# Kernel optimization log

Measured on AMD Instinct MI355X. Metric: run time of the kernel, lower is better.

## Reference

```python
import jax, jax.numpy as jnp
import numpy as np

N_NODES = 50000
N_EDGES = 600000
CLASSIC_DIM = 128
GRAPH_OUTPUT_DIM = 96
NUM_RELATIONS = 4


def setup_inputs() -> dict:
    key = jax.random.key(0)
    ks = jax.random.split(key, 10)
    x = jax.random.normal(ks[0], (N_NODES, CLASSIC_DIM), dtype=jnp.float32)
    edge_index = jax.random.randint(ks[1], (2, N_EDGES), 0, N_NODES, dtype=jnp.int64)
    edge_type = jax.random.randint(ks[2], (N_EDGES,), 0, NUM_RELATIONS, dtype=jnp.int64)
    s1 = 1.0 / np.sqrt(CLASSIC_DIM)
    W_root1 = jax.random.normal(ks[3], (CLASSIC_DIM, CLASSIC_DIM), dtype=jnp.float32) * s1
    W_rel1 = jax.random.normal(ks[4], (NUM_RELATIONS, CLASSIC_DIM, CLASSIC_DIM), dtype=jnp.float32) * s1
    b1 = jnp.zeros((CLASSIC_DIM,), dtype=jnp.float32)
    W_root2 = jax.random.normal(ks[5], (CLASSIC_DIM, GRAPH_OUTPUT_DIM), dtype=jnp.float32) * s1
    W_rel2 = jax.random.normal(ks[6], (NUM_RELATIONS, CLASSIC_DIM, GRAPH_OUTPUT_DIM), dtype=jnp.float32) * s1
    b2 = jnp.zeros((GRAPH_OUTPUT_DIM,), dtype=jnp.float32)
    return {"classic_features": x, "edge_index": edge_index, "edge_type": edge_type,
            "W_root1": W_root1, "W_rel1": W_rel1, "b1": b1,
            "W_root2": W_root2, "W_rel2": W_rel2, "b2": b2}


def _rgcn_layer(x, edge_index, edge_type, W_root, W_rel, b):
    # RGCN: h_i = W_root x_i + b + sum_r (1/deg_{i,r}) * W_r * sum_{j in N_r(i)} x_j
    # Aggregate-then-transform (valid by linearity) to keep the matmul small.
    src, dst = edge_index[0], edge_index[1]
    msgs = x[src]  # [E, d_in] irregular gather
    out = x @ W_root + b
    n = x.shape[0]
    num_rel = W_rel.shape[0]
    for r in range(num_rel):  # small fixed loop over relation types
        mask = (edge_type == r).astype(x.dtype)  # [E]
        agg = jax.ops.segment_sum(msgs * mask[:, None], dst, num_segments=n)  # [N, d_in]
        deg = jax.ops.segment_sum(mask, dst, num_segments=n)  # [N]
        agg = agg / jnp.maximum(deg, 1.0)[:, None]  # mean per relation (PyG default norm)
        out = out + agg @ W_rel[r]
    return out


def reference(classic_features, edge_index, edge_type, W_root1, W_rel1, b1, W_root2, W_rel2, b2):
    h = _rgcn_layer(classic_features, edge_index, edge_type, W_root1, W_rel1, b1)
    h = jax.nn.relu(h)
    # dropout(0.2) is identity in eval mode
    out = _rgcn_layer(h, edge_index, edge_type, W_root2, W_rel2, b2)
    return out
```

## Files before the change

kernel.cpp:

```cpp
#include <hip/hip_runtime.h>

#define DIM_IN 128
#define NREL 4
#define KTOT (DIM_IN + NREL * DIM_IN)
#define SCAN_CHUNK 1024

typedef __attribute__((ext_vector_type(8))) short short8;
typedef __attribute__((ext_vector_type(4))) float floatx4;

__device__ inline unsigned short f2bf(float f) {
    union { float f; unsigned int i; } c;
    c.f = f;
    unsigned int r = c.i + 0x7FFF + ((c.i >> 16) & 1);
    return (unsigned short)(r >> 16);
}
__device__ inline float bf2f(unsigned short u) {
    union { unsigned int i; float f; } c;
    c.i = ((unsigned int)u) << 16;
    return c.f;
}

__device__ inline void gload16_lds(const void* g, void* l) {
    __builtin_amdgcn_global_load_lds((const __attribute__((address_space(1))) unsigned int*)g,
                                     (__attribute__((address_space(3))) unsigned int*)l,
                                     16, 0, 0);
}

__global__ __launch_bounds__(256) void prep_kernel(
    const float* __restrict__ x, unsigned short* __restrict__ xb, int n4,
    const float* __restrict__ Wroot1, const float* __restrict__ Wrel1,
    unsigned short* __restrict__ Wt1,
    const float* __restrict__ Wroot2, const float* __restrict__ Wrel2,
    unsigned short* __restrict__ Wt2,
    const int* __restrict__ ei, const int* __restrict__ et,
    int* __restrict__ counts, int E) {
    int t = blockIdx.x * 256 + threadIdx.x;
    if (t < n4) {
        float4 v = ((const float4*)x)[t];
        ushort4 o;
        o.x = f2bf(v.x); o.y = f2bf(v.y); o.z = f2bf(v.z); o.w = f2bf(v.w);
        ((ushort4*)xb)[t] = o;
    }
    if (t < (128 + 96) * KTOT) {
        if (t < 128 * KTOT) {
            int n = t / KTOT, k = t - n * KTOT;
            float v = (k < DIM_IN) ? Wroot1[(size_t)k * 128 + n]
                                   : Wrel1[(size_t)(k - DIM_IN) * 128 + n];
            Wt1[t] = f2bf(v);
        } else {
            int t2 = t - 128 * KTOT;
            int n = t2 / KTOT, k = t2 - n * KTOT;
            float v = (k < DIM_IN) ? Wroot2[(size_t)k * 96 + n]
                                   : Wrel2[(size_t)(k - DIM_IN) * 96 + n];
            Wt2[t2] = f2bf(v);
        }
    }
    if (t < E) {
        atomicAdd(&counts[(size_t)ei[E + t] * NREL + et[t]], 1);
    }
}

__device__ int block_exscan256(int v) {
    __shared__ int tmp[256];
    int t = threadIdx.x;
    tmp[t] = v;
    __syncthreads();
    for (int d = 1; d < 256; d <<= 1) {
        int add = (t >= d) ? tmp[t - d] : 0;
        __syncthreads();
        tmp[t] += add;
        __syncthreads();
    }
    return tmp[t] - v;
}

__global__ __launch_bounds__(256) void scanA_kernel(const int* __restrict__ counts,
                                                    int* __restrict__ chunkTot, int nb) {
    int base = blockIdx.x * SCAN_CHUNK + threadIdx.x * 4;
    int s = 0;
#pragma unroll
    for (int i = 0; i < 4; i++) {
        int idx = base + i;
        s += (idx < nb) ? counts[idx] : 0;
    }
    __shared__ int red[256];
    red[threadIdx.x] = s;
    __syncthreads();
    for (int d = 128; d > 0; d >>= 1) {
        if (threadIdx.x < d) red[threadIdx.x] += red[threadIdx.x + d];
        __syncthreads();
    }
    if (threadIdx.x == 0) chunkTot[blockIdx.x] = red[0];
}

__global__ __launch_bounds__(256) void scanB_kernel(const int* __restrict__ chunkTot,
                                                    int* __restrict__ chunkBase, int nChunks) {
    int t = threadIdx.x;
    int v = (t < nChunks) ? chunkTot[t] : 0;
    int ex = block_exscan256(v);
    if (t < nChunks) chunkBase[t] = ex;
}

__global__ __launch_bounds__(256) void scanC_kernel(const int* __restrict__ counts,
                                                    const int* __restrict__ chunkBase,
                                                    int* __restrict__ offs,
                                                    int* __restrict__ cursor, int nb) {
    int base = blockIdx.x * SCAN_CHUNK + threadIdx.x * 4;
    int c[4], s = 0;
#pragma unroll
    for (int i = 0; i < 4; i++) {
        int idx = base + i;
        c[i] = (idx < nb) ? counts[idx] : 0;
        s += c[i];
    }
    int pos = block_exscan256(s) + chunkBase[blockIdx.x];
#pragma unroll
    for (int i = 0; i < 4; i++) {
        int idx = base + i;
        if (idx < nb) {
            offs[idx] = pos;
            cursor[idx] = pos;
        }
        pos += c[i];
    }
}

__global__ void place_kernel(const int* __restrict__ ei, const int* __restrict__ et,
                             int* __restrict__ cursor, int* __restrict__ csr, int E) {
    int e = blockIdx.x * 256 + threadIdx.x;
    if (e >= E) return;
    int b = ei[E + e] * NREL + et[e];
    int p = atomicAdd(&cursor[b], 1);
    csr[p] = ei[e];
}

__global__ __launch_bounds__(256) void agg_kernel(
    const unsigned short* __restrict__ feat, const int* __restrict__ csr,
    const int* __restrict__ offs, const int* __restrict__ counts,
    unsigned short* __restrict__ agg, int nb) {
    int l16 = threadIdx.x & 15;
    int g = (blockIdx.x * 256 + threadIdx.x) >> 4;
    if (g >= nb) return;
    int start = offs[g];
    int cnt = counts[g];
    float acc[8];
#pragma unroll
    for (int j = 0; j < 8; j++) acc[j] = 0.f;
    for (int base = 0; base < cnt; base += 16) {
        int m = cnt - base;
        if (m > 16) m = 16;
        int pick = (l16 < m) ? l16 : (m - 1);
        int idx = csr[start + base + pick];
        for (int j = 0; j < m; j++) {
            int s = __shfl(idx, j, 16);
            short8 u = *(const short8*)(feat + (size_t)s * DIM_IN + l16 * 8);
#pragma unroll
            for (int c = 0; c < 8; c++) acc[c] += bf2f((unsigned short)u[c]);
        }
    }
    float sc = (cnt > 0) ? (1.0f / (float)cnt) : 0.f;
    short8 o;
#pragma unroll
    for (int j = 0; j < 8; j++) o[j] = (short)f2bf(acc[j] * sc);
    *(short8*)(agg + (size_t)g * DIM_IN + l16 * 8) = o;
}

template <int NOUT, bool STORE_BF16_RELU>
__global__ __launch_bounds__(256) void mfma_gemm_kernel(
    const unsigned short* __restrict__ xb,
    const unsigned short* __restrict__ agg,
    const unsigned short* __restrict__ Wt,
    const float* __restrict__ bias,
    void* __restrict__ outp,
    int N) {
    constexpr int NT = NOUT / 32;
    constexpr int ACH = 128 * 8;
    constexpr int BCH = NOUT * 8;
    constexpr int APAN = 128 * 32;
    constexpr int BPAN = NOUT * 32;
    __shared__ unsigned short sA[2 * APAN];
    __shared__ unsigned short sB[2 * BPAN];
    const int t = threadIdx.x;
    const int w = t >> 6;
    const int lane = t & 63;
    const int q = lane >> 4;
    const int l15 = lane & 15;
    const int wm = w >> 1, wn = w & 1;
    const int m0 = blockIdx.x * 128;

    floatx4 acc[4][NT];
#pragma unroll
    for (int mt = 0; mt < 4; mt++)
#pragma unroll
        for (int nt = 0; nt < NT; nt++) acc[mt][nt] = (floatx4)0.f;

    for (int ks = 0; ks < KTOT / 64; ks++) {
        const int k0 = ks * 64;
#pragma unroll
        for (int r = 0; r < ACH / 256; r++) {
            int idx = t + r * 256;
            int panel = idx >> 9;
            int rem = idx & 511;
            int row = rem >> 2, ch = rem & 3;
            int rowg = m0 + row;
            if (rowg >= N) rowg = N - 1;
            int col = panel * 32 + ch * 8;
            const unsigned short* gp =
                (k0 < DIM_IN)
                    ? (xb + (size_t)rowg * DIM_IN + k0 + col)
                    : (agg + (size_t)rowg * (NREL * DIM_IN) + (k0 - DIM_IN) + col);
            gload16_lds(gp, sA + (size_t)idx * 8);
        }
#pragma unroll
        for (int r = 0; r < BCH / 256; r++) {
            int idx = t + r * 256;
            int panel = idx / (NOUT * 4);
            int rem = idx - panel * (NOUT * 4);
            int nrow = rem >> 2, ch = rem & 3;
            const unsigned short* gp = Wt + (size_t)nrow * KTOT + k0 + panel * 32 + ch * 8;
            gload16_lds(gp, sB + (size_t)idx * 8);
        }
        __syncthreads();
#pragma unroll
        for (int s = 0; s < 2; s++) {
            short8 aF[4], bF[NT];
#pragma unroll
            for (int mt = 0; mt < 4; mt++)
                aF[mt] = *(const short8*)(sA + s * APAN +
                                          (size_t)(wm * 64 + mt * 16 + l15) * 32 + q * 8);
#pragma unroll
            for (int nt = 0; nt < NT; nt++)
                bF[nt] = *(const short8*)(sB + s * BPAN +
                                          (size_t)(wn * (NOUT / 2) + nt * 16 + l15) * 32 + q * 8);
#pragma unroll
            for (int mt = 0; mt < 4; mt++)
#pragma unroll
                for (int nt = 0; nt < NT; nt++)
                    acc[mt][nt] = __builtin_amdgcn_mfma_f32_16x16x32_bf16(aF[mt], bF[nt],
                                                                          acc[mt][nt], 0, 0, 0);
        }
        __syncthreads();
    }

#pragma unroll
    for (int nt = 0; nt < NT; nt++) {
        int colg = wn * (NOUT / 2) + nt * 16 + l15;
        float bv = bias[colg];
#pragma unroll
        for (int mt = 0; mt < 4; mt++) {
            int rbase = m0 + wm * 64 + mt * 16 + q * 4;
#pragma unroll
            for (int r = 0; r < 4; r++) {
                int grow = rbase + r;
                if (grow < N) {
                    float v = acc[mt][nt][r] + bv;
                    if (STORE_BF16_RELU) {
                        v = fmaxf(v, 0.f);
                        ((unsigned short*)outp)[(size_t)grow * NOUT + colg] = f2bf(v);
                    } else {
                        ((float*)outp)[(size_t)grow * NOUT + colg] = v;
                    }
                }
            }
        }
    }
}

extern "C" void kernel_launch(void* const* d_in, const int* in_sizes, int n_in,
                              void* d_out, int out_size, void* d_ws, size_t ws_size,
                              hipStream_t stream) {
    const float* x = (const float*)d_in[0];
    const int* ei = (const int*)d_in[1];
    const int* et = (const int*)d_in[2];
    const float* Wroot1 = (const float*)d_in[3];
    const float* Wrel1 = (const float*)d_in[4];
    const float* b1 = (const float*)d_in[5];
    const float* Wroot2 = (const float*)d_in[6];
    const float* Wrel2 = (const float*)d_in[7];
    const float* b2 = (const float*)d_in[8];
    float* out = (float*)d_out;

    int N = in_sizes[0] / DIM_IN;
    int E = in_sizes[2];
    int nb = N * NREL;
    int nChunks = (nb + SCAN_CHUNK - 1) / SCAN_CHUNK;

    char* p = (char*)d_ws;
    unsigned short* xb = (unsigned short*)p;   p += (size_t)N * DIM_IN * 2;
    unsigned short* hb = (unsigned short*)p;   p += (size_t)N * DIM_IN * 2;
    unsigned short* agg = (unsigned short*)p;  p += (size_t)nb * DIM_IN * 2;
    unsigned short* Wt1 = (unsigned short*)p;  p += (size_t)128 * KTOT * 2;
    unsigned short* Wt2 = (unsigned short*)p;  p += (size_t)96 * KTOT * 2;
    int* counts = (int*)p;                     p += (size_t)nb * 4;
    int* offs = (int*)p;                       p += (size_t)nb * 4;
    int* cursor = (int*)p;                     p += (size_t)nb * 4;
    int* chunkTot = (int*)p;                   p += 256 * 4;
    int* chunkBase = (int*)p;                  p += 256 * 4;
    int* csr = (int*)p;                        p += (size_t)E * 4;
    if ((size_t)(p - (char*)d_ws) > ws_size) return;

    int n4 = N * DIM_IN / 4;
    int prepWork = n4;
    if (prepWork < E) prepWork = E;
    if (prepWork < (128 + 96) * KTOT) prepWork = (128 + 96) * KTOT;

    hipMemsetAsync(counts, 0, (size_t)nb * sizeof(int), stream);
    prep_kernel<<<(prepWork + 255) / 256, 256, 0, stream>>>(
        x, xb, n4, Wroot1, Wrel1, Wt1, Wroot2, Wrel2, Wt2, ei, et, counts, E);
    scanA_kernel<<<nChunks, 256, 0, stream>>>(counts, chunkTot, nb);
    scanB_kernel<<<1, 256, 0, stream>>>(chunkTot, chunkBase, nChunks);
    scanC_kernel<<<nChunks, 256, 0, stream>>>(counts, chunkBase, offs, cursor, nb);
    place_kernel<<<(E + 255) / 256, 256, 0, stream>>>(ei, et, cursor, csr, E);

    int gAgg = (nb * 16 + 255) / 256;
    int gB = (N + 127) / 128;
    agg_kernel<<<gAgg, 256, 0, stream>>>(xb, csr, offs, counts, agg, nb);
    mfma_gemm_kernel<128, true><<<gB, 256, 0, stream>>>(xb, agg, Wt1, b1, hb, N);
    agg_kernel<<<gAgg, 256, 0, stream>>>(hb, csr, offs, counts, agg, nb);
    mfma_gemm_kernel<96, false><<<gB, 256, 0, stream>>>(hb, agg, Wt2, b2, out, N);
}
```

Baseline: 262.3 us.

## Switch RGCN layers to transform-then-aggregate with per-node gather over packed CSR

Each layer now first multiplies node features by the concatenated root and relation weights (N x 128 times 128 x 5C), then a gather kernel sums each destination's neighbours from the transformed relation slices, scaled by the inverse per-relation degree, on top of the root term. Edge relation ids are packed into the CSR source index so one pass per node covers all relations. The place atomics now advance the offset array in place, and the prefix shifted by one element recovers segment starts. This removes the N*4*128 aggregated intermediate and the long-K GEMM, but the GEMM output grows to 5C columns per node, and gathers read C-wide rows with fewer active lanes when C is 96.

```diff
diff --git a/kernel.cpp b/kernel.cpp
--- a/kernel.cpp
+++ b/kernel.cpp
@@ -2,8 +2,8 @@
 
 #define DIM_IN 128
 #define NREL 4
-#define KTOT (DIM_IN + NREL * DIM_IN)
 #define SCAN_CHUNK 1024
+#define SRC_MASK 0xFFFFF
 
 typedef __attribute__((ext_vector_type(8))) short short8;
 typedef __attribute__((ext_vector_type(4))) float floatx4;
@@ -41,17 +41,23 @@
         o.x = f2bf(v.x); o.y = f2bf(v.y); o.z = f2bf(v.z); o.w = f2bf(v.w);
         ((ushort4*)xb)[t] = o;
     }
-    if (t < (128 + 96) * KTOT) {
-        if (t < 128 * KTOT) {
-            int n = t / KTOT, k = t - n * KTOT;
-            float v = (k < DIM_IN) ? Wroot1[(size_t)k * 128 + n]
-                                   : Wrel1[(size_t)(k - DIM_IN) * 128 + n];
+    if (t < (640 + 480) * 128) {
+        if (t < 640 * 128) {
+            int n = t >> 7, k = t & 127;
+            float v = (n < 128) ? Wroot1[(size_t)k * 128 + n]
+                                : Wrel1[(size_t)((((n - 128) >> 7) * 128) + k) * 128 +
+                                        ((n - 128) & 127)];
             Wt1[t] = f2bf(v);
         } else {
-            int t2 = t - 128 * KTOT;
-            int n = t2 / KTOT, k = t2 - n * KTOT;
-            float v = (k < DIM_IN) ? Wroot2[(size_t)k * 96 + n]
-                                   : Wrel2[(size_t)(k - DIM_IN) * 96 + n];
+            int t2 = t - 640 * 128;
+            int n = t2 >> 7, k = t2 & 127;
+            float v;
+            if (n < 96) {
+                v = Wroot2[(size_t)k * 96 + n];
+            } else {
+                int q = n - 96, r = q / 96, c = q - r * 96;
+                v = Wrel2[(size_t)(r * 128 + k) * 96 + c];
+            }
             Wt2[t2] = f2bf(v);
         }
     }
@@ -94,17 +100,18 @@
 }
 
 __global__ __launch_bounds__(256) void scanB_kernel(const int* __restrict__ chunkTot,
-                                                    int* __restrict__ chunkBase, int nChunks) {
+                                                    int* __restrict__ chunkBase, int nChunks,
+                                                    int* __restrict__ curM1) {
     int t = threadIdx.x;
     int v = (t < nChunks) ? chunkTot[t] : 0;
     int ex = block_exscan256(v);
     if (t < nChunks) chunkBase[t] = ex;
+    if (t == 0) curM1[0] = 0;
 }
 
 __global__ __launch_bounds__(256) void scanC_kernel(const int* __restrict__ counts,
                                                     const int* __restrict__ chunkBase,
-                                                    int* __restrict__ offs,
-                                                    int* __restrict__ cursor, int nb) {
+                                                    int* __restrict__ cur, int nb) {
     int base = blockIdx.x * SCAN_CHUNK + threadIdx.x * 4;
     int c[4], s = 0;
 #pragma unroll
@@ -117,76 +124,59 @@
 #pragma unroll
     for (int i = 0; i < 4; i++) {
         int idx = base + i;
-        if (idx < nb) {
-            offs[idx] = pos;
-            cursor[idx] = pos;
-        }
+        if (idx < nb) cur[idx] = pos;
         pos += c[i];
     }
 }
 
 __global__ void place_kernel(const int* __restrict__ ei, const int* __restrict__ et,
-                             int* __restrict__ cursor, int* __restrict__ csr, int E) {
+                             int* __restrict__ cur, int* __restrict__ csr, int E) {
     int e = blockIdx.x * 256 + threadIdx.x;
     if (e >= E) return;
-    int b = ei[E + e] * NREL + et[e];
-    int p = atomicAdd(&cursor[b], 1);
-    csr[p] = ei[e];
-}
-
-__global__ __launch_bounds__(256) void agg_kernel(
-    const unsigned short* __restrict__ feat, const int* __restrict__ csr,
-    const int* __restrict__ offs, const int* __restrict__ counts,
-    unsigned short* __restrict__ agg, int nb) {
-    int l16 = threadIdx.x & 15;
-    int g = (blockIdx.x * 256 + threadIdx.x) >> 4;
-    if (g >= nb) return;
-    int start = offs[g];
-    int cnt = counts[g];
-    float acc[8];
-#pragma unroll
-    for (int j = 0; j < 8; j++) acc[j] = 0.f;
-    for (int base = 0; base < cnt; base += 16) {
-        int m = cnt - base;
-        if (m > 16) m = 16;
-        int pick = (l16 < m) ? l16 : (m - 1);
-        int idx = csr[start + base + pick];
-        for (int j = 0; j < m; j++) {
-            int s = __shfl(idx, j, 16);
-            short8 u = *(const short8*)(feat + (size_t)s * DIM_IN + l16 * 8);
-#pragma unroll
-            for (int c = 0; c < 8; c++) acc[c] += bf2f((unsigned short)u[c]);
-        }
-    }
-    float sc = (cnt > 0) ? (1.0f / (float)cnt) : 0.f;
-    short8 o;
-#pragma unroll
-    for (int j = 0; j < 8; j++) o[j] = (short)f2bf(acc[j] * sc);
-    *(short8*)(agg + (size_t)g * DIM_IN + l16 * 8) = o;
-}
-
-template <int NOUT, bool STORE_BF16_RELU>
-__global__ __launch_bounds__(256) void mfma_gemm_kernel(
-    const unsigned short* __restrict__ xb,
-    const unsigned short* __restrict__ agg,
+    int r = et[e];
+    int b = ei[E + e] * NREL + r;
+    int p = atomicAdd(&cur[b], 1);
+    csr[p] = ei[e] | (r << 20);
+}
+
+template <int CH, int NTOT>
+__global__ __launch_bounds__(256) void gemm_tf_kernel(
+    const unsigned short* __restrict__ A,
     const unsigned short* __restrict__ Wt,
     const float* __restrict__ bias,
-    void* __restrict__ outp,
+    unsigned short* __restrict__ y,
     int N) {
-    constexpr int NT = NOUT / 32;
-    constexpr int ACH = 128 * 8;
-    constexpr int BCH = NOUT * 8;
-    constexpr int APAN = 128 * 32;
-    constexpr int BPAN = NOUT * 32;
-    __shared__ unsigned short sA[2 * APAN];
-    __shared__ unsigned short sB[2 * BPAN];
+    constexpr int NT = CH / 32;
+    constexpr int BCHP = CH * 4;
+    __shared__ unsigned short sA[128 * 128];
+    __shared__ unsigned short sB[CH * 128];
     const int t = threadIdx.x;
     const int w = t >> 6;
     const int lane = t & 63;
     const int q = lane >> 4;
     const int l15 = lane & 15;
     const int wm = w >> 1, wn = w & 1;
-    const int m0 = blockIdx.x * 128;
+    const int m0 = blockIdx.y * 128;
+    const int c0 = blockIdx.x * CH;
+
+#pragma unroll
+    for (int r = 0; r < 8; r++) {
+        int idx = t + r * 256;
+        int panel = idx >> 9, rem = idx & 511;
+        int row = rem >> 2, ch = rem & 3;
+        int rowg = m0 + row;
+        if (rowg >= N) rowg = N - 1;
+        gload16_lds(A + (size_t)rowg * 128 + panel * 32 + ch * 8, sA + (size_t)idx * 8);
+    }
+#pragma unroll
+    for (int r = 0; r < (CH * 16) / 256; r++) {
+        int idx = t + r * 256;
+        int panel = idx / BCHP, rem = idx - panel * BCHP;
+        int nrow = rem >> 2, ch = rem & 3;
+        gload16_lds(Wt + (size_t)(c0 + nrow) * 128 + panel * 32 + ch * 8,
+                    sB + (size_t)idx * 8);
+    }
+    __syncthreads();
 
     floatx4 acc[4][NT];
 #pragma unroll
@@ -194,74 +184,114 @@
 #pragma unroll
         for (int nt = 0; nt < NT; nt++) acc[mt][nt] = (floatx4)0.f;
 
-    for (int ks = 0; ks < KTOT / 64; ks++) {
-        const int k0 = ks * 64;
-#pragma unroll
-        for (int r = 0; r < ACH / 256; r++) {
-            int idx = t + r * 256;
-            int panel = idx >> 9;
-            int rem = idx & 511;
-            int row = rem >> 2, ch = rem & 3;
-            int rowg = m0 + row;
-            if (rowg >= N) rowg = N - 1;
-            int col = panel * 32 + ch * 8;
-            const unsigned short* gp =
-                (k0 < DIM_IN)
-                    ? (xb + (size_t)rowg * DIM_IN + k0 + col)
-                    : (agg + (size_t)rowg * (NREL * DIM_IN) + (k0 - DIM_IN) + col);
-            gload16_lds(gp, sA + (size_t)idx * 8);
-        }
-#pragma unroll
-        for (int r = 0; r < BCH / 256; r++) {
-            int idx = t + r * 256;
-            int panel = idx / (NOUT * 4);
-            int rem = idx - panel * (NOUT * 4);
-            int nrow = rem >> 2, ch = rem & 3;
-            const unsigned short* gp = Wt + (size_t)nrow * KTOT + k0 + panel * 32 + ch * 8;
-            gload16_lds(gp, sB + (size_t)idx * 8);
-        }
-        __syncthreads();
-#pragma unroll
-        for (int s = 0; s < 2; s++) {
-            short8 aF[4], bF[NT];
-#pragma unroll
-            for (int mt = 0; mt < 4; mt++)
-                aF[mt] = *(const short8*)(sA + s * APAN +
-                                          (size_t)(wm * 64 + mt * 16 + l15) * 32 + q * 8);
+#pragma unroll
+    for (int s = 0; s < 4; s++) {
+        short8 aF[4], bF[NT];
+#pragma unroll
+        for (int mt = 0; mt < 4; mt++)
+            aF[mt] = *(const short8*)(sA + s * 4096 + (size_t)(wm * 64 + mt * 16 + l15) * 32 + q * 8);
+#pragma unroll
+        for (int nt = 0; nt < NT; nt++)
+            bF[nt] = *(const short8*)(sB + s * (CH * 32) +
+                                      (size_t)(wn * (CH / 2) + nt * 16 + l15) * 32 + q * 8);
+#pragma unroll
+        for (int mt = 0; mt < 4; mt++)
 #pragma unroll
             for (int nt = 0; nt < NT; nt++)
-                bF[nt] = *(const short8*)(sB + s * BPAN +
-                                          (size_t)(wn * (NOUT / 2) + nt * 16 + l15) * 32 + q * 8);
-#pragma unroll
-            for (int mt = 0; mt < 4; mt++)
-#pragma unroll
-                for (int nt = 0; nt < NT; nt++)
-                    acc[mt][nt] = __builtin_amdgcn_mfma_f32_16x16x32_bf16(aF[mt], bF[nt],
-                                                                          acc[mt][nt], 0, 0, 0);
-        }
-        __syncthreads();
+                acc[mt][nt] =
+                    __builtin_amdgcn_mfma_f32_16x16x32_bf16(aF[mt], bF[nt], acc[mt][nt], 0, 0, 0);
     }
 
 #pragma unroll
     for (int nt = 0; nt < NT; nt++) {
-        int colg = wn * (NOUT / 2) + nt * 16 + l15;
-        float bv = bias[colg];
+        int colc = wn * (CH / 2) + nt * 16 + l15;
+        int colg = c0 + colc;
+        float bv = (blockIdx.x == 0) ? bias[colc] : 0.f;
 #pragma unroll
         for (int mt = 0; mt < 4; mt++) {
             int rbase = m0 + wm * 64 + mt * 16 + q * 4;
 #pragma unroll
             for (int r = 0; r < 4; r++) {
                 int grow = rbase + r;
-                if (grow < N) {
-                    float v = acc[mt][nt][r] + bv;
-                    if (STORE_BF16_RELU) {
-                        v = fmaxf(v, 0.f);
-                        ((unsigned short*)outp)[(size_t)grow * NOUT + colg] = f2bf(v);
-                    } else {
-                        ((float*)outp)[(size_t)grow * NOUT + colg] = v;
-                    }
-                }
+                if (grow < N)
+                    y[(size_t)grow * NTOT + colg] = f2bf(acc[mt][nt][r] + bv);
             }
+        }
+    }
+}
+
+template <int NTOT, int ROOTC, bool RELU_BF16>
+__global__ __launch_bounds__(256) void gather_kernel(
+    const unsigned short* __restrict__ y, const int* __restrict__ csr,
+    const int* __restrict__ cur, void* __restrict__ outp, int N) {
+    constexpr int AL = ROOTC / 8;
+    const int l = threadIdx.x & 15;
+    const int dst = (blockIdx.x * 256 + threadIdx.x) >> 4;
+    if (dst >= N) return;
+    const int g0 = dst * NREL;
+    int o0 = cur[g0 - 1], o1 = cur[g0], o2 = cur[g0 + 1], o3 = cur[g0 + 2], o4 = cur[g0 + 3];
+    float sc0 = (o1 > o0) ? 1.f / (float)(o1 - o0) : 0.f;
+    float sc1 = (o2 > o1) ? 1.f / (float)(o2 - o1) : 0.f;
+    float sc2 = (o3 > o2) ? 1.f / (float)(o3 - o2) : 0.f;
+    float sc3 = (o4 > o3) ? 1.f / (float)(o4 - o3) : 0.f;
+    int tot = o4 - o0;
+
+    float acc[8];
+    if (l < AL) {
+        short8 rt = *(const short8*)(y + (size_t)dst * NTOT + l * 8);
+#pragma unroll
+        for (int c = 0; c < 8; c++) acc[c] = bf2f((unsigned short)rt[c]);
+    } else {
+#pragma unroll
+        for (int c = 0; c < 8; c++) acc[c] = 0.f;
+    }
+
+    for (int b0 = 0; b0 < tot; b0 += 16) {
+        int m = tot - b0;
+        if (m > 16) m = 16;
+        int pick = (l < m) ? l : (m - 1);
+        int pv = csr[o0 + b0 + pick];
+        int j = 0;
+        for (; j + 1 < m; j += 2) {
+            int v0 = __shfl(pv, j, 16);
+            int v1 = __shfl(pv, j + 1, 16);
+            int s0 = v0 & SRC_MASK, r0 = v0 >> 20;
+            int s1 = v1 & SRC_MASK, r1 = v1 >> 20;
+            float f0 = (r0 == 0) ? sc0 : (r0 == 1) ? sc1 : (r0 == 2) ? sc2 : sc3;
+            float f1 = (r1 == 0) ? sc0 : (r1 == 1) ? sc1 : (r1 == 2) ? sc2 : sc3;
+            if (l < AL) {
+                short8 u0 = *(const short8*)(y + (size_t)s0 * NTOT + ROOTC + r0 * ROOTC + l * 8);
+                short8 u1 = *(const short8*)(y + (size_t)s1 * NTOT + ROOTC + r1 * ROOTC + l * 8);
+#pragma unroll
+                for (int c = 0; c < 8; c++) acc[c] += f0 * bf2f((unsigned short)u0[c]);
+#pragma unroll
+                for (int c = 0; c < 8; c++) acc[c] += f1 * bf2f((unsigned short)u1[c]);
+            }
+        }
+        if (j < m) {
+            int v0 = __shfl(pv, j, 16);
+            int s0 = v0 & SRC_MASK, r0 = v0 >> 20;
+            float f0 = (r0 == 0) ? sc0 : (r0 == 1) ? sc1 : (r0 == 2) ? sc2 : sc3;
+            if (l < AL) {
+                short8 u0 = *(const short8*)(y + (size_t)s0 * NTOT + ROOTC + r0 * ROOTC + l * 8);
+#pragma unroll
+                for (int c = 0; c < 8; c++) acc[c] += f0 * bf2f((unsigned short)u0[c]);
+            }
+        }
+    }
+
+    if (l < AL) {
+        if (RELU_BF16) {
+            short8 o;
+#pragma unroll
+            for (int c = 0; c < 8; c++) o[c] = (short)f2bf(fmaxf(acc[c], 0.f));
+            *(short8*)((unsigned short*)outp + (size_t)dst * ROOTC + l * 8) = o;
+        } else {
+            float4 a = make_float4(acc[0], acc[1], acc[2], acc[3]);
+            float4 b = make_float4(acc[4], acc[5], acc[6], acc[7]);
+            float4* op = (float4*)((float*)outp + (size_t)dst * ROOTC + l * 8);
+            op[0] = a;
+            op[1] = b;
         }
     }
 }
@@ -286,36 +316,37 @@
     int nChunks = (nb + SCAN_CHUNK - 1) / SCAN_CHUNK;
 
     char* p = (char*)d_ws;
-    unsigned short* xb = (unsigned short*)p;   p += (size_t)N * DIM_IN * 2;
-    unsigned short* hb = (unsigned short*)p;   p += (size_t)N * DIM_IN * 2;
-    unsigned short* agg = (unsigned short*)p;  p += (size_t)nb * DIM_IN * 2;
-    unsigned short* Wt1 = (unsigned short*)p;  p += (size_t)128 * KTOT * 2;
-    unsigned short* Wt2 = (unsigned short*)p;  p += (size_t)96 * KTOT * 2;
+    unsigned short* xb = (unsigned short*)p;   p += (size_t)N * 128 * 2;
+    unsigned short* hb = (unsigned short*)p;   p += (size_t)N * 128 * 2;
+    unsigned short* y1 = (unsigned short*)p;   p += (size_t)N * 640 * 2;
+    unsigned short* y2 = (unsigned short*)p;   p += (size_t)N * 480 * 2;
+    unsigned short* Wt1 = (unsigned short*)p;  p += (size_t)640 * 128 * 2;
+    unsigned short* Wt2 = (unsigned short*)p;  p += (size_t)480 * 128 * 2;
     int* counts = (int*)p;                     p += (size_t)nb * 4;
-    int* offs = (int*)p;                       p += (size_t)nb * 4;
-    int* cursor = (int*)p;                     p += (size_t)nb * 4;
+    int* curBuf = (int*)p;                     p += ((size_t)nb + 1) * 4;
     int* chunkTot = (int*)p;                   p += 256 * 4;
     int* chunkBase = (int*)p;                  p += 256 * 4;
     int* csr = (int*)p;                        p += (size_t)E * 4;
     if ((size_t)(p - (char*)d_ws) > ws_size) return;
-
-    int n4 = N * DIM_IN / 4;
+    int* cur = curBuf + 1;
+
+    int n4 = N * 128 / 4;
     int prepWork = n4;
     if (prepWork < E) prepWork = E;
-    if (prepWork < (128 + 96) * KTOT) prepWork = (128 + 96) * KTOT;
+    if (prepWork < (640 + 480) * 128) prepWork = (640 + 480) * 128;
 
     hipMemsetAsync(counts, 0, (size_t)nb * sizeof(int), stream);
     prep_kernel<<<(prepWork + 255) / 256, 256, 0, stream>>>(
         x, xb, n4, Wroot1, Wrel1, Wt1, Wroot2, Wrel2, Wt2, ei, et, counts, E);
     scanA_kernel<<<nChunks, 256, 0, stream>>>(counts, chunkTot, nb);
-    scanB_kernel<<<1, 256, 0, stream>>>(chunkTot, chunkBase, nChunks);
-    scanC_kernel<<<nChunks, 256, 0, stream>>>(counts, chunkBase, offs, cursor, nb);
-    place_kernel<<<(E + 255) / 256, 256, 0, stream>>>(ei, et, cursor, csr, E);
-
-    int gAgg = (nb * 16 + 255) / 256;
-    int gB = (N + 127) / 128;
-    agg_kernel<<<gAgg, 256, 0, stream>>>(xb, csr, offs, counts, agg, nb);
-    mfma_gemm_kernel<128, true><<<gB, 256, 0, stream>>>(xb, agg, Wt1, b1, hb, N);
-    agg_kernel<<<gAgg, 256, 0, stream>>>(hb, csr, offs, counts, agg, nb);
-    mfma_gemm_kernel<96, false><<<gB, 256, 0, stream>>>(hb, agg, Wt2, b2, out, N);
-}
+    scanB_kernel<<<1, 256, 0, stream>>>(chunkTot, chunkBase, nChunks, curBuf);
+    scanC_kernel<<<nChunks, 256, 0, stream>>>(counts, chunkBase, cur, nb);
+    place_kernel<<<(E + 255) / 256, 256, 0, stream>>>(ei, et, cur, csr, E);
+
+    int gM = (N + 127) / 128;
+    int gG = (N * 16 + 255) / 256;
+    gemm_tf_kernel<128, 640><<<dim3(5, gM), 256, 0, stream>>>(xb, Wt1, b1, y1, N);
+    gather_kernel<640, 128, true><<<gG, 256, 0, stream>>>(y1, csr, cur, hb, N);
+    gemm_tf_kernel<96, 480><<<dim3(5, gM), 256, 0, stream>>>(hb, Wt2, b2, y2, N);
+    gather_kernel<480, 96, false><<<gG, 256, 0, stream>>>(y2, csr, cur, out, N);
+}
```

Result: slower. 299.4 us (+14.2%).

## Fuse neighbor aggregation into GEMM A-tile loading and drop agg buffer

Applied to the files above, without the earlier changes.

Removes the separate aggregation kernels and the intermediate per-relation aggregate buffer. The GEMM now builds the relation A-tiles on the fly by gathering neighbor rows through the CSR and averaging them in registers before writing to LDS. After place_kernel the post-atomic cursor array doubles as the end-offset array, with a leading zero slot so cur[g-1] gives the start, which removes the separate offs buffer. This trades a global write and read of the aggregate for irregular gathers done inside the GEMM with only 8 lanes per row. That leaves far fewer threads doing the gathers, exposes their latency, and puts the gather on the GEMM's critical path.

```diff
diff --git a/kernel.cpp b/kernel.cpp
--- a/kernel.cpp
+++ b/kernel.cpp
@@ -41,19 +41,17 @@
         o.x = f2bf(v.x); o.y = f2bf(v.y); o.z = f2bf(v.z); o.w = f2bf(v.w);
         ((ushort4*)xb)[t] = o;
     }
-    if (t < (128 + 96) * KTOT) {
-        if (t < 128 * KTOT) {
-            int n = t / KTOT, k = t - n * KTOT;
-            float v = (k < DIM_IN) ? Wroot1[(size_t)k * 128 + n]
-                                   : Wrel1[(size_t)(k - DIM_IN) * 128 + n];
-            Wt1[t] = f2bf(v);
-        } else {
-            int t2 = t - 128 * KTOT;
-            int n = t2 / KTOT, k = t2 - n * KTOT;
-            float v = (k < DIM_IN) ? Wroot2[(size_t)k * 96 + n]
-                                   : Wrel2[(size_t)(k - DIM_IN) * 96 + n];
-            Wt2[t2] = f2bf(v);
-        }
+    if (t < 128 * KTOT) {
+        int n = t / KTOT, k = t - n * KTOT;
+        float v = (k < DIM_IN) ? Wroot1[(size_t)k * 128 + n]
+                               : Wrel1[(size_t)(k - DIM_IN) * 128 + n];
+        Wt1[t] = f2bf(v);
+    }
+    if (t < 96 * KTOT) {
+        int n = t / KTOT, k = t - n * KTOT;
+        float v = (k < DIM_IN) ? Wroot2[(size_t)k * 96 + n]
+                               : Wrel2[(size_t)(k - DIM_IN) * 96 + n];
+        Wt2[t] = f2bf(v);
     }
     if (t < E) {
         atomicAdd(&counts[(size_t)ei[E + t] * NREL + et[t]], 1);
@@ -94,17 +92,18 @@
 }
 
 __global__ __launch_bounds__(256) void scanB_kernel(const int* __restrict__ chunkTot,
-                                                    int* __restrict__ chunkBase, int nChunks) {
+                                                    int* __restrict__ chunkBase, int nChunks,
+                                                    int* __restrict__ curM1) {
     int t = threadIdx.x;
     int v = (t < nChunks) ? chunkTot[t] : 0;
     int ex = block_exscan256(v);
     if (t < nChunks) chunkBase[t] = ex;
+    if (t == 0) curM1[0] = 0;
 }
 
 __global__ __launch_bounds__(256) void scanC_kernel(const int* __restrict__ counts,
                                                     const int* __restrict__ chunkBase,
-                                                    int* __restrict__ offs,
-                                                    int* __restrict__ cursor, int nb) {
+                                                    int* __restrict__ cur, int nb) {
     int base = blockIdx.x * SCAN_CHUNK + threadIdx.x * 4;
     int c[4], s = 0;
 #pragma unroll
@@ -117,65 +116,30 @@
 #pragma unroll
     for (int i = 0; i < 4; i++) {
         int idx = base + i;
-        if (idx < nb) {
-            offs[idx] = pos;
-            cursor[idx] = pos;
-        }
+        if (idx < nb) cur[idx] = pos;
         pos += c[i];
     }
 }
 
 __global__ void place_kernel(const int* __restrict__ ei, const int* __restrict__ et,
-                             int* __restrict__ cursor, int* __restrict__ csr, int E) {
+                             int* __restrict__ cur, int* __restrict__ csr, int E) {
     int e = blockIdx.x * 256 + threadIdx.x;
     if (e >= E) return;
     int b = ei[E + e] * NREL + et[e];
-    int p = atomicAdd(&cursor[b], 1);
+    int p = atomicAdd(&cur[b], 1);
     csr[p] = ei[e];
 }
 
-__global__ __launch_bounds__(256) void agg_kernel(
-    const unsigned short* __restrict__ feat, const int* __restrict__ csr,
-    const int* __restrict__ offs, const int* __restrict__ counts,
-    unsigned short* __restrict__ agg, int nb) {
-    int l16 = threadIdx.x & 15;
-    int g = (blockIdx.x * 256 + threadIdx.x) >> 4;
-    if (g >= nb) return;
-    int start = offs[g];
-    int cnt = counts[g];
-    float acc[8];
-#pragma unroll
-    for (int j = 0; j < 8; j++) acc[j] = 0.f;
-    for (int base = 0; base < cnt; base += 16) {
-        int m = cnt - base;
-        if (m > 16) m = 16;
-        int pick = (l16 < m) ? l16 : (m - 1);
-        int idx = csr[start + base + pick];
-        for (int j = 0; j < m; j++) {
-            int s = __shfl(idx, j, 16);
-            short8 u = *(const short8*)(feat + (size_t)s * DIM_IN + l16 * 8);
-#pragma unroll
-            for (int c = 0; c < 8; c++) acc[c] += bf2f((unsigned short)u[c]);
-        }
-    }
-    float sc = (cnt > 0) ? (1.0f / (float)cnt) : 0.f;
-    short8 o;
-#pragma unroll
-    for (int j = 0; j < 8; j++) o[j] = (short)f2bf(acc[j] * sc);
-    *(short8*)(agg + (size_t)g * DIM_IN + l16 * 8) = o;
-}
-
 template <int NOUT, bool STORE_BF16_RELU>
-__global__ __launch_bounds__(256) void mfma_gemm_kernel(
+__global__ __launch_bounds__(256) void gemm_fused_kernel(
     const unsigned short* __restrict__ xb,
-    const unsigned short* __restrict__ agg,
     const unsigned short* __restrict__ Wt,
+    const int* __restrict__ csr,
+    const int* __restrict__ cur,
     const float* __restrict__ bias,
     void* __restrict__ outp,
     int N) {
     constexpr int NT = NOUT / 32;
-    constexpr int ACH = 128 * 8;
-    constexpr int BCH = NOUT * 8;
     constexpr int APAN = 128 * 32;
     constexpr int BPAN = NOUT * 32;
     __shared__ unsigned short sA[2 * APAN];
@@ -187,6 +151,8 @@
     const int l15 = lane & 15;
     const int wm = w >> 1, wn = w & 1;
     const int m0 = blockIdx.x * 128;
+    const int grp = t >> 3;
+    const int gl = t & 7;
 
     floatx4 acc[4][NT];
 #pragma unroll
@@ -196,29 +162,52 @@
 
     for (int ks = 0; ks < KTOT / 64; ks++) {
         const int k0 = ks * 64;
-#pragma unroll
-        for (int r = 0; r < ACH / 256; r++) {
-            int idx = t + r * 256;
-            int panel = idx >> 9;
-            int rem = idx & 511;
-            int row = rem >> 2, ch = rem & 3;
-            int rowg = m0 + row;
-            if (rowg >= N) rowg = N - 1;
-            int col = panel * 32 + ch * 8;
-            const unsigned short* gp =
-                (k0 < DIM_IN)
-                    ? (xb + (size_t)rowg * DIM_IN + k0 + col)
-                    : (agg + (size_t)rowg * (NREL * DIM_IN) + (k0 - DIM_IN) + col);
-            gload16_lds(gp, sA + (size_t)idx * 8);
+        if (k0 < DIM_IN) {
+#pragma unroll
+            for (int r = 0; r < 4; r++) {
+                int idx = t + r * 256;
+                int panel = idx >> 9, rem = idx & 511;
+                int row = rem >> 2, ch = rem & 3;
+                int rowg = m0 + row;
+                if (rowg >= N) rowg = N - 1;
+                gload16_lds(xb + (size_t)rowg * DIM_IN + k0 + panel * 32 + ch * 8,
+                            sA + (size_t)idx * 8);
+            }
+        } else {
+            const int koff = k0 - DIM_IN;
+            const int rel = koff >> 7;
+            const int kbase = koff & 127;
+#pragma unroll
+            for (int p = 0; p < 4; p++) {
+                int row = p * 32 + grp;
+                int dstg = m0 + row;
+                if (dstg >= N) dstg = N - 1;
+                int g = dstg * NREL + rel;
+                int s0 = cur[g - 1], e0 = cur[g];
+                float facc[8];
+#pragma unroll
+                for (int c = 0; c < 8; c++) facc[c] = 0.f;
+                for (int i = s0; i < e0; i++) {
+                    int src = csr[i];
+                    short8 u = *(const short8*)(xb + (size_t)src * DIM_IN + kbase + gl * 8);
+#pragma unroll
+                    for (int c = 0; c < 8; c++) facc[c] += bf2f((unsigned short)u[c]);
+                }
+                float sc = (e0 > s0) ? (1.0f / (float)(e0 - s0)) : 0.f;
+                short8 o;
+#pragma unroll
+                for (int c = 0; c < 8; c++) o[c] = (short)f2bf(facc[c] * sc);
+                *(short8*)(sA + (gl >> 2) * APAN + (size_t)row * 32 + (gl & 3) * 8) = o;
+            }
         }
 #pragma unroll
-        for (int r = 0; r < BCH / 256; r++) {
+        for (int r = 0; r < (NOUT * 8) / 256; r++) {
             int idx = t + r * 256;
             int panel = idx / (NOUT * 4);
             int rem = idx - panel * (NOUT * 4);
             int nrow = rem >> 2, ch = rem & 3;
-            const unsigned short* gp = Wt + (size_t)nrow * KTOT + k0 + panel * 32 + ch * 8;
-            gload16_lds(gp, sB + (size_t)idx * 8);
+            gload16_lds(Wt + (size_t)nrow * KTOT + k0 + panel * 32 + ch * 8,
+                        sB + (size_t)idx * 8);
         }
         __syncthreads();
 #pragma unroll
@@ -288,34 +277,30 @@
     char* p = (char*)d_ws;
     unsigned short* xb = (unsigned short*)p;   p += (size_t)N * DIM_IN * 2;
     unsigned short* hb = (unsigned short*)p;   p += (size_t)N * DIM_IN * 2;
-    unsigned short* agg = (unsigned short*)p;  p += (size_t)nb * DIM_IN * 2;
     unsigned short* Wt1 = (unsigned short*)p;  p += (size_t)128 * KTOT * 2;
     unsigned short* Wt2 = (unsigned short*)p;  p += (size_t)96 * KTOT * 2;
     int* counts = (int*)p;                     p += (size_t)nb * 4;
-    int* offs = (int*)p;                       p += (size_t)nb * 4;
-    int* cursor = (int*)p;                     p += (size_t)nb * 4;
+    int* curBuf = (int*)p;                     p += ((size_t)nb + 1) * 4;
     int* chunkTot = (int*)p;                   p += 256 * 4;
     int* chunkBase = (int*)p;                  p += 256 * 4;
     int* csr = (int*)p;                        p += (size_t)E * 4;
     if ((size_t)(p - (char*)d_ws) > ws_size) return;
+    int* cur = curBuf + 1;
 
     int n4 = N * DIM_IN / 4;
     int prepWork = n4;
     if (prepWork < E) prepWork = E;
-    if (prepWork < (128 + 96) * KTOT) prepWork = (128 + 96) * KTOT;
+    if (prepWork < 128 * KTOT) prepWork = 128 * KTOT;
 
     hipMemsetAsync(counts, 0, (size_t)nb * sizeof(int), stream);
     prep_kernel<<<(prepWork + 255) / 256, 256, 0, stream>>>(
         x, xb, n4, Wroot1, Wrel1, Wt1, Wroot2, Wrel2, Wt2, ei, et, counts, E);
     scanA_kernel<<<nChunks, 256, 0, stream>>>(counts, chunkTot, nb);
-    scanB_kernel<<<1, 256, 0, stream>>>(chunkTot, chunkBase, nChunks);
-    scanC_kernel<<<nChunks, 256, 0, stream>>>(counts, chunkBase, offs, cursor, nb);
-    place_kernel<<<(E + 255) / 256, 256, 0, stream>>>(ei, et, cursor, csr, E);
-
-    int gAgg = (nb * 16 + 255) / 256;
+    scanB_kernel<<<1, 256, 0, stream>>>(chunkTot, chunkBase, nChunks, curBuf);
+    scanC_kernel<<<nChunks, 256, 0, stream>>>(counts, chunkBase, cur, nb);
+    place_kernel<<<(E + 255) / 256, 256, 0, stream>>>(ei, et, cur, csr, E);
+
     int gB = (N + 127) / 128;
-    agg_kernel<<<gAgg, 256, 0, stream>>>(xb, csr, offs, counts, agg, nb);
-    mfma_gemm_kernel<128, true><<<gB, 256, 0, stream>>>(xb, agg, Wt1, b1, hb, N);
-    agg_kernel<<<gAgg, 256, 0, stream>>>(hb, csr, offs, counts, agg, nb);
-    mfma_gemm_kernel<96, false><<<gB, 256, 0, stream>>>(hb, agg, Wt2, b2, out, N);
-}
+    gemm_fused_kernel<128, true><<<gB, 256, 0, stream>>>(xb, Wt1, csr, cur, b1, hb, N);
+    gemm_fused_kernel<96, false><<<gB, 256, 0, stream>>>(hb, Wt2, csr, cur, b2, out, N);
+}
```

Measured after the change: 460.2 us. 1.75x slower.
